# Kernel optimization log

Hardware: AMD Instinct MI355X
Metric: run time of the kernel (lower is better)

Reference implementation:

```python
import jax, jax.numpy as jnp
import numpy as np

ITER = 50
SMOOTH = 1e-05


def _max_pool(x, window):
    # x: [B, C, D, H, W]; 'same' max pool with stride 1, -inf padding
    # (matches torch F.max_pool3d semantics with symmetric padding).
    win = (1, 1) + window
    pads = [(0, 0), (0, 0)] + [((w - 1) // 2, (w - 1) // 2) for w in window]
    return jax.lax.reduce_window(x, -jnp.inf, jax.lax.max, win, (1,) * 5, pads)


def soft_erode(img):
    p1 = -_max_pool(-img, (3, 1, 1))
    p2 = -_max_pool(-img, (1, 3, 1))
    p3 = -_max_pool(-img, (1, 1, 3))
    return jnp.minimum(jnp.minimum(p1, p2), p3)


def soft_dilate(img):
    return _max_pool(img, (3, 3, 3))


def soft_open(img):
    return soft_dilate(soft_erode(img))


def soft_skel(img, n_iter):
    skel = jax.nn.relu(img - soft_open(img))

    def body(_, carry):
        img, skel = carry
        img = soft_erode(img)
        delta = jax.nn.relu(img - soft_open(img))
        skel = skel + jax.nn.relu(delta - skel * delta)
        return (img, skel)

    _, skel = jax.lax.fori_loop(0, n_iter, body, (img, skel))
    return skel


def setup_inputs() -> dict:
    key = jax.random.key(0)
    k1, k2 = jax.random.split(key)
    shape = (2, 2, 96, 192, 192)
    pred = jax.random.uniform(k1, shape, dtype=jnp.float32)
    target = jax.random.uniform(k2, shape, dtype=jnp.float32)
    return {"pred": pred, "target": target}


def reference(pred, target):
    pred_fg = pred[:, 1:2, ...]
    target_fg = target[:, 1:2, ...].astype(jnp.float32)
    skel_pred = soft_skel(pred_fg, ITER)
    skel_target = soft_skel(target_fg, ITER)
    tprec = (jnp.sum(skel_pred * target_fg) + SMOOTH) / (jnp.sum(skel_pred) + SMOOTH)
    tsens = (jnp.sum(skel_target * pred_fg) + SMOOTH) / (jnp.sum(skel_target) + SMOOTH)
    cl_dice = 2.0 * (tprec * tsens) / (tprec + tsens + SMOOTH)
    return 1.0 - cl_dice
```

## Files before the change

### kernel.cpp

```cpp
#include <hip/hip_runtime.h>
#include <math.h>

#define NX 192
#define NY 192
#define NZ 96
#define NV 4
#define VOL (NZ * NY * NX)
#define NTOT (NV * VOL)
#define YS NX
#define ZS (NY * NX)

#define TX 48
#define TY 16
#define ZCH 24
#define NG 14
#define AROWS (TY + 4)
#define EROWS (TY + 2)
#define AJOBS (AROWS * NG)
#define EJOBS (EROWS * NG)
#define UJOBS (TY * (TX / 4))

#define TY2 12
#define ZCH2 16
#define R2A 18

#define SLOT5(x) (((x) + 100) % 5)
#define SLOT3(x) (((x) + 99) % 3)
#define SLOT2(x) (((x) + 100) % 2)

#define HINF  0x7C00u
#define HNINF 0xFC00u

typedef _Float16 h2v __attribute__((ext_vector_type(2)));

struct __align__(8) H4u { unsigned lo, hi; };

__device__ __forceinline__ h2v h2_of(unsigned u) { return __builtin_bit_cast(h2v, u); }
__device__ __forceinline__ unsigned u_of(h2v h) { return __builtin_bit_cast(unsigned, h); }

__device__ __forceinline__ H4u h4min(H4u a, H4u b) {
    H4u r;
    r.lo = u_of(__builtin_elementwise_min(h2_of(a.lo), h2_of(b.lo)));
    r.hi = u_of(__builtin_elementwise_min(h2_of(a.hi), h2_of(b.hi)));
    return r;
}
__device__ __forceinline__ H4u h4max(H4u a, H4u b) {
    H4u r;
    r.lo = u_of(__builtin_elementwise_max(h2_of(a.lo), h2_of(b.lo)));
    r.hi = u_of(__builtin_elementwise_max(h2_of(a.hi), h2_of(b.hi)));
    return r;
}
__device__ __forceinline__ H4u shl1(H4u c, unsigned p16) {
    H4u r;
    r.lo = (c.lo << 16) | (p16 & 0xFFFFu);
    r.hi = (c.hi << 16) | (c.lo >> 16);
    return r;
}
__device__ __forceinline__ H4u shr1(H4u c, unsigned n16) {
    H4u r;
    r.lo = (c.lo >> 16) | (c.hi << 16);
    r.hi = (c.hi >> 16) | ((n16 & 0xFFFFu) << 16);
    return r;
}
__device__ __forceinline__ H4u f4_to_h4(float4 f) {
    h2v a, b;
    a[0] = (_Float16)f.x; a[1] = (_Float16)f.y;
    b[0] = (_Float16)f.z; b[1] = (_Float16)f.w;
    H4u r; r.lo = u_of(a); r.hi = u_of(b); return r;
}
__device__ __forceinline__ float4 h4_to_f4(H4u h) {
    h2v a = h2_of(h.lo), b = h2_of(h.hi);
    return make_float4((float)a[0], (float)a[1], (float)b[0], (float)b[1]);
}

__device__ __forceinline__ float4 min4(float4 a, float4 b) {
    return make_float4(fminf(a.x, b.x), fminf(a.y, b.y),
                       fminf(a.z, b.z), fminf(a.w, b.w));
}
__device__ __forceinline__ float4 max4(float4 a, float4 b) {
    return make_float4(fmaxf(a.x, b.x), fmaxf(a.y, b.y),
                       fmaxf(a.z, b.z), fmaxf(a.w, b.w));
}
__device__ __forceinline__ float4 win3max(float a, float4 b, float c) {
    return make_float4(fmaxf(fmaxf(a, b.x), b.y),
                       fmaxf(fmaxf(b.x, b.y), b.z),
                       fmaxf(fmaxf(b.y, b.z), b.w),
                       fmaxf(fmaxf(b.z, b.w), c));
}

template<bool FIRST>
__global__ __launch_bounds__(256, 6) void fused2_kernel(
    const float* __restrict__ pred, const float* __restrict__ target,
    const _Float16* __restrict__ Ain, _Float16* __restrict__ Eout,
    _Float16* __restrict__ skel)
{
    __shared__ H4u As[5][R2A][NG];
    __shared__ H4u E1c[3][16][NG];
    __shared__ H4u ZM1[2][16][NG];
    __shared__ H4u ZM2[2][16][NG];

    const int tid = threadIdx.x;
    const int lr  = tid >> 4;
    const int c   = tid & 15;
    const int cc  = (c < 14) ? c : 13;
    const int sr  = tid / 14;
    const int sg  = tid - sr * 14;

    const int x0 = blockIdx.x * TX;
    const int y0 = blockIdx.y * TY2;
    const int v  = blockIdx.z / 6;
    const int ch = blockIdx.z % 6;
    const int z0 = ch * ZCH2;
    const int z1 = z0 + ZCH2;

    const float* Af = nullptr;
    const _Float16* Ah = nullptr;
    if (FIRST) Af = ((v < 2) ? pred : target) + (size_t)((v & 1) * 2 + 1) * VOL;
    else       Ah = Ain + (size_t)v * VOL;
    _Float16* Ev = Eout + (size_t)v * VOL;
    _Float16* Sv = skel + (size_t)v * VOL;

    const H4u HP4 = { 0x7C007C00u, 0x7C007C00u };
    const H4u HN4 = { 0xFC00FC00u, 0xFC00FC00u };
    const float4 ZERO4 = make_float4(0.f, 0.f, 0.f, 0.f);

    const bool xlo = (x0 == 0);
    const bool xhi = (x0 + TX == NX);

    const int  gys  = y0 - 3 + sr;
    const int  gxs  = x0 - 4 + 4 * sg;
    const bool stIn = (sr < R2A) && (gys >= 0) && (gys < NY) &&
                      (gxs >= 0) && (gxs < NX);

    const int  gx   = x0 - 4 + 4 * c;
    const bool gxin = (c < 14) && (gx >= 0) && (gx < NX);
    const int  gyo  = y0 - 2 + lr;
    const bool yIn  = (gyo >= 0) && (gyo < NY);
    const bool uAct = (lr >= 2 && lr <= 13 && c >= 1 && c <= 12);
    const int  rdn  = (lr > 0) ? lr - 1 : 0;
    const int  rup  = (lr < 15) ? lr + 1 : 15;

    auto stageLoad = [&](int za) -> H4u {
        H4u val = HP4;
        if (stIn && za >= 0 && za < NZ) {
            if (FIRST)
                val = f4_to_h4(*(const float4*)(Af + (size_t)za * ZS + gys * YS + gxs));
            else
                val = *(const H4u*)(Ah + (size_t)za * ZS + gys * YS + gxs);
        }
        return val;
    };
    auto stageWrite = [&](int za, H4u val) {
        if (sr < R2A) As[SLOT5(za)][sr][sg] = val;
    };

    auto e1compute = [&](int zp) -> H4u {
        if (zp >= NZ) return HP4;
        const int s_c = SLOT5(zp), s_m = SLOT5(zp - 1), s_p = SLOT5(zp + 1);
        const bool hp = (zp + 1 < NZ);
        const int ar = lr + 1;
        H4u cen = As[s_c][ar][cc];
        H4u ylo = As[s_c][ar - 1][cc];
        H4u yhi = As[s_c][ar + 1][cc];
        H4u zlo = As[s_m][ar][cc];
        H4u zhi = hp ? As[s_p][ar][cc] : HP4;
        unsigned lw = __shfl_up(cen.hi, 1) >> 16;
        unsigned rx = __shfl_down(cen.lo, 1) & 0xFFFFu;
        if (c == 0) lw = HINF;
        H4u m = h4min(cen, shl1(cen, lw));
        m = h4min(m, shr1(cen, rx));
        m = h4min(m, h4min(ylo, yhi));
        m = h4min(m, h4min(zlo, zhi));
        if (zp < 0 || !yIn || !gxin) m = HP4;
        if (c < 14) E1c[SLOT3(zp)][lr][c] = m;
        return m;
    };

    stageWrite(z0 - 3, stageLoad(z0 - 3));
    stageWrite(z0 - 2, stageLoad(z0 - 2));
    stageWrite(z0 - 1, stageLoad(z0 - 1));
    stageWrite(z0,     stageLoad(z0));
    stageWrite(z0 + 1, stageLoad(z0 + 1));
    __syncthreads();
    H4u e1m2 = e1compute(z0 - 2);
    H4u e1m1 = e1compute(z0 - 1);
    __syncthreads();
    stageWrite(z0 + 2, stageLoad(z0 + 2));
    H4u e1c = e1compute(z0);
    __syncthreads();

    H4u e1m3 = HP4;
    H4u e2c = HN4, e2m1 = HN4;
    H4u zm1_prev = HN4, zm2_prev = HN4;
    float4 skA = ZERO4, sq1 = ZERO4, sq2 = ZERO4;

    for (int z = z0; z <= z1 + 2; ++z) {
        const bool doStage = (z <= z1 - 1);
        H4u stv = doStage ? stageLoad(z + 3) : HP4;
        float4 skN = ZERO4;
        if (!FIRST && z < z1 && uAct)
            skN = h4_to_f4(*(const H4u*)(Sv + (size_t)z * ZS + gyo * YS + gx));

        H4u e1new = (z + 1 <= z1 + 1) ? e1compute(z + 1) : HP4;

        H4u zm1w;
        {
            H4u t0 = (z >= 1) ? e1m1 : HN4;
            H4u t2 = (z + 1 < NZ) ? e1new : HN4;
            zm1w = h4max(t0, h4max(e1c, t2));
            if (!yIn || !gxin) zm1w = HN4;
            if (c < 14) ZM1[SLOT2(z)][lr][c] = zm1w;
        }

        const int p = z - 1;
        H4u e2new = HN4;
        if (p >= 0 && p <= z1 && p < NZ) {
            H4u cen = e1m1;
            H4u zlo = e1m2;
            H4u zhi = e1c;
            H4u ylo = E1c[SLOT3(p)][rdn][cc];
            H4u yhi = E1c[SLOT3(p)][rup][cc];
            unsigned lwE = __shfl_up(cen.hi, 1) >> 16;
            unsigned rxE = __shfl_down(cen.lo, 1) & 0xFFFFu;
            if (c == 0) lwE = HINF;
            H4u m2 = h4min(cen, shl1(cen, lwE));
            m2 = h4min(m2, shr1(cen, rxE));
            m2 = h4min(m2, h4min(ylo, yhi));
            m2 = h4min(m2, h4min(zlo, zhi));
            if (yIn && gxin) {
                e2new = m2;
                if (p >= z0 && p < z1 && lr >= 2 && lr <= 13 && c >= 1 && c <= 12)
                    *(H4u*)(Ev + (size_t)p * ZS + gyo * YS + gx) = m2;
            }
        }

        H4u zm2w = h4max(e2m1, h4max(e2c, e2new));
        if (c < 14) ZM2[SLOT2(z - 2)][lr][c] = zm2w;

        float4 spnew = ZERO4;
        if (p >= z0 && p < z1) {
            H4u vm = h4max(ZM1[SLOT2(p)][rdn][cc],
                     h4max(zm1_prev, ZM1[SLOT2(p)][rup][cc]));
            unsigned lw = __shfl_up(vm.hi, 1) >> 16;
            unsigned rx = __shfl_down(vm.lo, 1) & 0xFFFFu;
            if (xlo && c == 1)  lw = HNINF;
            if (xhi && c == 12) rx = HNINF;
            if (uAct) {
                H4u dilh = h4max(h4max(shl1(vm, lw), vm), shr1(vm, rx));
                float4 dil = h4_to_f4(dilh);
                float4 a = h4_to_f4(As[SLOT5(p)][lr + 1][cc]);
                float4 s = skA;
                float dd;
                dd = fmaxf(a.x - dil.x, 0.f); s.x += fmaxf(dd - s.x * dd, 0.f);
                dd = fmaxf(a.y - dil.y, 0.f); s.y += fmaxf(dd - s.y * dd, 0.f);
                dd = fmaxf(a.z - dil.z, 0.f); s.z += fmaxf(dd - s.z * dd, 0.f);
                dd = fmaxf(a.w - dil.w, 0.f); s.w += fmaxf(dd - s.w * dd, 0.f);
                spnew = s;
            }
        }

        const int q = z - 3;
        if (q >= z0 && q < z1) {
            H4u vm2 = h4max(ZM2[SLOT2(q)][rdn][cc],
                      h4max(zm2_prev, ZM2[SLOT2(q)][rup][cc]));
            unsigned lw = __shfl_up(vm2.hi, 1) >> 16;
            unsigned rx = __shfl_down(vm2.lo, 1) & 0xFFFFu;
            if (xlo && c == 1)  lw = HNINF;
            if (xhi && c == 12) rx = HNINF;
            if (uAct) {
                H4u dilh = h4max(h4max(shl1(vm2, lw), vm2), shr1(vm2, rx));
                float4 dil = h4_to_f4(dilh);
                float4 a = h4_to_f4(e1m3);
                float4 s = sq2;
                float dd;
                dd = fmaxf(a.x - dil.x, 0.f); s.x += fmaxf(dd - s.x * dd, 0.f);
                dd = fmaxf(a.y - dil.y, 0.f); s.y += fmaxf(dd - s.y * dd, 0.f);
                dd = fmaxf(a.z - dil.z, 0.f); s.z += fmaxf(dd - s.z * dd, 0.f);
                dd = fmaxf(a.w - dil.w, 0.f); s.w += fmaxf(dd - s.w * dd, 0.f);
                *(H4u*)(Sv + (size_t)q * ZS + gyo * YS + gx) = f4_to_h4(s);
            }
        }

        if (doStage) stageWrite(z + 3, stv);

        __syncthreads();
        e1m3 = e1m2; e1m2 = e1m1; e1m1 = e1c; e1c = e1new;
        e2m1 = e2c; e2c = e2new;
        zm1_prev = zm1w; zm2_prev = zm2w;
        sq2 = sq1; sq1 = spnew; skA = skN;
    }
}

__global__ __launch_bounds__(256, 3) void fused_last_kernel(
    const _Float16* __restrict__ Ain,
    const float* __restrict__ pred, const float* __restrict__ target,
    const _Float16* __restrict__ skel, double* __restrict__ sums)
{
    __shared__ float4 As[4][AROWS][NG];
    __shared__ float4 Es[3][EROWS][NG];
    __shared__ float4 Ms[EROWS][NG];
    __shared__ double sred[8];

    const int tid = threadIdx.x;
    const int x0 = blockIdx.x * TX;
    const int y0 = blockIdx.y * TY;
    const int v  = blockIdx.z >> 2;
    const int z0 = (blockIdx.z & 3) * ZCH;
    const int z1 = z0 + ZCH;

    const _Float16* Av = Ain + (size_t)v * VOL;
    const _Float16* Sv = skel + (size_t)v * VOL;
    const float* Ov = ((v < 2) ? target : pred) + (size_t)((v & 1) * 2 + 1) * VOL;

    const float4 PINF4 = make_float4(INFINITY, INFINITY, INFINITY, INFINITY);
    const float4 NINF4 = make_float4(-INFINITY, -INFINITY, -INFINITY, -INFINITY);
    const float4 ZERO4 = make_float4(0.f, 0.f, 0.f, 0.f);

    const int ur  = tid / (TX / 4);
    const int ugp = tid - ur * (TX / 4);

    auto stageA = [&](int z) {
        int slot = (z + 8) & 3;
        float4* dst = &As[slot][0][0];
        if (z < 0 || z >= NZ) {
            for (int j = tid; j < AJOBS; j += 256) dst[j] = PINF4;
        } else {
            const _Float16* P = Av + (size_t)z * ZS;
            for (int j = tid; j < AJOBS; j += 256) {
                int r = j / NG, g = j - r * NG;
                int gy = y0 - 2 + r;
                int gx0 = x0 - 4 + 4 * g;
                float4 val = PINF4;
                if (gy >= 0 && gy < NY && gx0 >= 0 && gx0 < NX)
                    val = h4_to_f4(*(const H4u*)(P + gy * YS + gx0));
                dst[j] = val;
            }
        }
    };

    auto eplane = [&](int z) {
        int es = (z + 9) % 3;
        float4* dst = &Es[es][0][0];
        if (z < 0 || z >= NZ) {
            for (int j = tid; j < EJOBS; j += 256) dst[j] = NINF4;
            return;
        }
        const int sc = (z + 8) & 3;
        const int sm = (z + 7) & 3;
        const int sp = (z + 9) & 3;
        for (int j = tid; j < EJOBS; j += 256) {
            int r = j / NG, g = j - r * NG;
            float4 c  = As[sc][r + 1][g];
            float4 yl = As[sc][r][g];
            float4 yh = As[sc][r + 2][g];
            float4 zl = As[sm][r + 1][g];
            float4 zh = As[sp][r + 1][g];
            float pw = (g > 0)      ? As[sc][r + 1][g - 1].w : INFINITY;
            float nx = (g < NG - 1) ? As[sc][r + 1][g + 1].x : INFINITY;
            float4 xl = make_float4(pw, c.x, c.y, c.z);
            float4 xr = make_float4(c.y, c.z, c.w, nx);
            float4 m = min4(c, xl);
            m = min4(m, xr);
            m = min4(m, yl);
            m = min4(m, yh);
            m = min4(m, zl);
            m = min4(m, zh);
            int gy = y0 - 1 + r;
            int gx0 = x0 - 4 + 4 * g;
            if (gy < 0 || gy >= NY || gx0 < 0 || gx0 >= NX) m = NINF4;
            dst[j] = m;
        }
    };

    stageA(z0 - 2); stageA(z0 - 1); stageA(z0); stageA(z0 + 1);
    __syncthreads();
    eplane(z0 - 1);
    eplane(z0);
    __syncthreads();
    stageA(z0 + 2);
    __syncthreads();

    double afd = 0.0, afs = 0.0;

    for (int z = z0; z < z1; ++z) {
        float4 oCur = ZERO4;
        if (tid < UJOBS)
            oCur = *(const float4*)(Ov + (size_t)z * ZS +
                                    (size_t)(y0 + ur) * YS + (x0 + ugp * 4));
        stageA(z + 3);
        eplane(z + 1);
        __syncthreads();
        {
            const float4* e0 = &Es[(z + 8) % 3][0][0];
            const float4* e1 = &Es[(z + 9) % 3][0][0];
            const float4* e2 = &Es[(z + 10) % 3][0][0];
            float4* mm = &Ms[0][0];
            for (int j = tid; j < EJOBS; j += 256)
                mm[j] = max4(max4(e0[j], e1[j]), e2[j]);
        }
        __syncthreads();
        if (tid < UJOBS) {
            int g = ugp + 1;
            float4 d = NINF4;
#pragma unroll
            for (int dy = 0; dy < 3; ++dy) {
                float a  = Ms[ur + dy][g - 1].w;
                float4 b = Ms[ur + dy][g];
                float cx = Ms[ur + dy][g + 1].x;
                d = max4(d, win3max(a, b, cx));
            }
            float4 av = As[(z + 8) & 3][ur + 2][g];
            float4 delta = make_float4(fmaxf(av.x - d.x, 0.0f),
                                       fmaxf(av.y - d.y, 0.0f),
                                       fmaxf(av.z - d.z, 0.0f),
                                       fmaxf(av.w - d.w, 0.0f));
            size_t gi = (size_t)z * ZS + (size_t)(y0 + ur) * YS + (x0 + ugp * 4);
            float4 s = h4_to_f4(*(const H4u*)(Sv + gi));
            s.x += fmaxf(delta.x - s.x * delta.x, 0.0f);
            s.y += fmaxf(delta.y - s.y * delta.y, 0.0f);
            s.z += fmaxf(delta.z - s.z * delta.z, 0.0f);
            s.w += fmaxf(delta.w - s.w * delta.w, 0.0f);
            afd += (double)(s.x * oCur.x + s.y * oCur.y +
                            s.z * oCur.z + s.w * oCur.w);
            afs += (double)(s.x + s.y + s.z + s.w);
        }
        __syncthreads();
    }

#pragma unroll
    for (int off = 32; off > 0; off >>= 1) {
        afd += __shfl_down(afd, off, 64);
        afs += __shfl_down(afs, off, 64);
    }
    int lane = tid & 63, wid = tid >> 6;
    if (lane == 0) { sred[wid * 2] = afd; sred[wid * 2 + 1] = afs; }
    __syncthreads();
    if (tid == 0) {
        double fd = sred[0] + sred[2] + sred[4] + sred[6];
        double fs = sred[1] + sred[3] + sred[5] + sred[7];
        if (v < 2) { atomicAdd(&sums[0], fd); atomicAdd(&sums[1], fs); }
        else       { atomicAdd(&sums[2], fd); atomicAdd(&sums[3], fs); }
    }
}

__global__ void final_kernel(const double* __restrict__ sums,
                             float* __restrict__ out) {
    if (threadIdx.x == 0 && blockIdx.x == 0) {
        const double SM = 1e-5;
        double tprec = (sums[0] + SM) / (sums[1] + SM);
        double tsens = (sums[2] + SM) / (sums[3] + SM);
        double cl = 2.0 * tprec * tsens / (tprec + tsens + SM);
        out[0] = (float)(1.0 - cl);
    }
}

extern "C" void kernel_launch(void* const* d_in, const int* in_sizes, int n_in,
                              void* d_out, int out_size, void* d_ws, size_t ws_size,
                              hipStream_t stream) {
    const float* pred = (const float*)d_in[0];
    const float* target = (const float*)d_in[1];
    float* out = (float*)d_out;

    _Float16* H0 = (_Float16*)d_ws;
    _Float16* H1 = H0 + NTOT;
    _Float16* skel = H1 + NTOT;
    double* sums = (double*)(skel + NTOT);

    hipMemsetAsync(sums, 0, 4 * sizeof(double), stream);

    dim3 dgrid(NX / TX, NY / TY2, NV * 6);
    dim3 fgrid(NX / TX, NY / TY, NV * 4);

    fused2_kernel<true><<<dgrid, 256, 0, stream>>>(pred, target, H0, H0, skel);
    _Float16* A = H0;
    _Float16* B = H1;
    for (int j = 0; j < 24; ++j) {
        fused2_kernel<false><<<dgrid, 256, 0, stream>>>(pred, target, A, B, skel);
        _Float16* t = A; A = B; B = t;
    }
    fused_last_kernel<<<fgrid, 256, 0, stream>>>(A, pred, target, skel, sums);

    final_kernel<<<1, 64, 0, stream>>>(sums, out);
}
```

Baseline: 1.705 ms.

## Compute skeleton update in packed fp16 and rewrite last kernel as register-streaming

```diff
diff --git a/kernel.cpp b/kernel.cpp
--- a/kernel.cpp
+++ b/kernel.cpp
@@ -11,20 +11,12 @@
 #define ZS (NY * NX)
 
 #define TX 48
-#define TY 16
-#define ZCH 24
-#define NG 14
-#define AROWS (TY + 4)
-#define EROWS (TY + 2)
-#define AJOBS (AROWS * NG)
-#define EJOBS (EROWS * NG)
-#define UJOBS (TY * (TX / 4))
-
 #define TY2 12
 #define ZCH2 16
+#define NG 14
 #define R2A 18
 
-#define SLOT5(x) (((x) + 100) % 5)
+#define SLOT4(x) (((x) + 100) % 4)
 #define SLOT3(x) (((x) + 99) % 3)
 #define SLOT2(x) (((x) + 100) % 2)
 
@@ -49,6 +41,31 @@
     r.lo = u_of(__builtin_elementwise_max(h2_of(a.lo), h2_of(b.lo)));
     r.hi = u_of(__builtin_elementwise_max(h2_of(a.hi), h2_of(b.hi)));
     return r;
+}
+__device__ __forceinline__ H4u h4add(H4u a, H4u b) {
+    H4u r;
+    r.lo = u_of(h2_of(a.lo) + h2_of(b.lo));
+    r.hi = u_of(h2_of(a.hi) + h2_of(b.hi));
+    return r;
+}
+__device__ __forceinline__ H4u h4sub(H4u a, H4u b) {
+    H4u r;
+    r.lo = u_of(h2_of(a.lo) - h2_of(b.lo));
+    r.hi = u_of(h2_of(a.hi) - h2_of(b.hi));
+    return r;
+}
+__device__ __forceinline__ H4u h4mul(H4u a, H4u b) {
+    H4u r;
+    r.lo = u_of(h2_of(a.lo) * h2_of(b.lo));
+    r.hi = u_of(h2_of(a.hi) * h2_of(b.hi));
+    return r;
+}
+__device__ __forceinline__ H4u h4skel(H4u s, H4u a, H4u dil) {
+    const H4u HZ4 = { 0u, 0u };
+    const H4u HONE = { 0x3C003C00u, 0x3C003C00u };
+    H4u dd = h4max(h4sub(a, dil), HZ4);
+    H4u t = h4mul(dd, h4sub(HONE, s));
+    return h4add(s, h4max(t, HZ4));
 }
 __device__ __forceinline__ H4u shl1(H4u c, unsigned p16) {
     H4u r;
@@ -71,21 +88,6 @@
 __device__ __forceinline__ float4 h4_to_f4(H4u h) {
     h2v a = h2_of(h.lo), b = h2_of(h.hi);
     return make_float4((float)a[0], (float)a[1], (float)b[0], (float)b[1]);
-}
-
-__device__ __forceinline__ float4 min4(float4 a, float4 b) {
-    return make_float4(fminf(a.x, b.x), fminf(a.y, b.y),
-                       fminf(a.z, b.z), fminf(a.w, b.w));
-}
-__device__ __forceinline__ float4 max4(float4 a, float4 b) {
-    return make_float4(fmaxf(a.x, b.x), fmaxf(a.y, b.y),
-                       fmaxf(a.z, b.z), fmaxf(a.w, b.w));
-}
-__device__ __forceinline__ float4 win3max(float a, float4 b, float c) {
-    return make_float4(fmaxf(fmaxf(a, b.x), b.y),
-                       fmaxf(fmaxf(b.x, b.y), b.z),
-                       fmaxf(fmaxf(b.y, b.z), b.w),
-                       fmaxf(fmaxf(b.z, b.w), c));
 }
 
 template<bool FIRST>
@@ -94,7 +96,7 @@
     const _Float16* __restrict__ Ain, _Float16* __restrict__ Eout,
     _Float16* __restrict__ skel)
 {
-    __shared__ H4u As[5][R2A][NG];
+    __shared__ H4u As[4][R2A][NG];
     __shared__ H4u E1c[3][16][NG];
     __shared__ H4u ZM1[2][16][NG];
     __shared__ H4u ZM2[2][16][NG];
@@ -122,7 +124,7 @@
 
     const H4u HP4 = { 0x7C007C00u, 0x7C007C00u };
     const H4u HN4 = { 0xFC00FC00u, 0xFC00FC00u };
-    const float4 ZERO4 = make_float4(0.f, 0.f, 0.f, 0.f);
+    const H4u HZ4 = { 0u, 0u };
 
     const bool xlo = (x0 == 0);
     const bool xhi = (x0 + TX == NX);
@@ -151,12 +153,12 @@
         return val;
     };
     auto stageWrite = [&](int za, H4u val) {
-        if (sr < R2A) As[SLOT5(za)][sr][sg] = val;
-    };
-
-    auto e1compute = [&](int zp) -> H4u {
-        if (zp >= NZ) return HP4;
-        const int s_c = SLOT5(zp), s_m = SLOT5(zp - 1), s_p = SLOT5(zp + 1);
+        if (sr < R2A) As[SLOT4(za)][sr][sg] = val;
+    };
+
+    auto e1compute = [&](int zp, H4u& cenOut) -> H4u {
+        if (zp >= NZ) { cenOut = HP4; return HP4; }
+        const int s_c = SLOT4(zp), s_m = SLOT4(zp - 1), s_p = SLOT4(zp + 1);
         const bool hp = (zp + 1 < NZ);
         const int ar = lr + 1;
         H4u cen = As[s_c][ar][cc];
@@ -164,6 +166,7 @@
         H4u yhi = As[s_c][ar + 1][cc];
         H4u zlo = As[s_m][ar][cc];
         H4u zhi = hp ? As[s_p][ar][cc] : HP4;
+        cenOut = cen;
         unsigned lw = __shfl_up(cen.hi, 1) >> 16;
         unsigned rx = __shfl_down(cen.lo, 1) & 0xFFFFu;
         if (c == 0) lw = HINF;
@@ -180,28 +183,31 @@
     stageWrite(z0 - 2, stageLoad(z0 - 2));
     stageWrite(z0 - 1, stageLoad(z0 - 1));
     stageWrite(z0,     stageLoad(z0));
+    __syncthreads();
+    H4u aT, a1, a2 = HP4;
+    H4u e1m2 = e1compute(z0 - 2, aT);
+    H4u e1m1 = e1compute(z0 - 1, aT);
+    __syncthreads();
     stageWrite(z0 + 1, stageLoad(z0 + 1));
     __syncthreads();
-    H4u e1m2 = e1compute(z0 - 2);
-    H4u e1m1 = e1compute(z0 - 1);
-    __syncthreads();
+    H4u e1c = e1compute(z0, a1);
     stageWrite(z0 + 2, stageLoad(z0 + 2));
-    H4u e1c = e1compute(z0);
     __syncthreads();
 
     H4u e1m3 = HP4;
     H4u e2c = HN4, e2m1 = HN4;
     H4u zm1_prev = HN4, zm2_prev = HN4;
-    float4 skA = ZERO4, sq1 = ZERO4, sq2 = ZERO4;
+    H4u skA = HZ4, sq1 = HZ4, sq2 = HZ4;
 
     for (int z = z0; z <= z1 + 2; ++z) {
         const bool doStage = (z <= z1 - 1);
         H4u stv = doStage ? stageLoad(z + 3) : HP4;
-        float4 skN = ZERO4;
+        H4u skN = HZ4;
         if (!FIRST && z < z1 && uAct)
-            skN = h4_to_f4(*(const H4u*)(Sv + (size_t)z * ZS + gyo * YS + gx));
-
-        H4u e1new = (z + 1 <= z1 + 1) ? e1compute(z + 1) : HP4;
+            skN = *(const H4u*)(Sv + (size_t)z * ZS + gyo * YS + gx);
+
+        H4u aC = HP4;
+        H4u e1new = (z <= z1) ? e1compute(z + 1, aC) : HP4;
 
         H4u zm1w;
         {
@@ -237,7 +243,7 @@
         H4u zm2w = h4max(e2m1, h4max(e2c, e2new));
         if (c < 14) ZM2[SLOT2(z - 2)][lr][c] = zm2w;
 
-        float4 spnew = ZERO4;
+        H4u spnew = HZ4;
         if (p >= z0 && p < z1) {
             H4u vm = h4max(ZM1[SLOT2(p)][rdn][cc],
                      h4max(zm1_prev, ZM1[SLOT2(p)][rup][cc]));
@@ -247,15 +253,7 @@
             if (xhi && c == 12) rx = HNINF;
             if (uAct) {
                 H4u dilh = h4max(h4max(shl1(vm, lw), vm), shr1(vm, rx));
-                float4 dil = h4_to_f4(dilh);
-                float4 a = h4_to_f4(As[SLOT5(p)][lr + 1][cc]);
-                float4 s = skA;
-                float dd;
-                dd = fmaxf(a.x - dil.x, 0.f); s.x += fmaxf(dd - s.x * dd, 0.f);
-                dd = fmaxf(a.y - dil.y, 0.f); s.y += fmaxf(dd - s.y * dd, 0.f);
-                dd = fmaxf(a.z - dil.z, 0.f); s.z += fmaxf(dd - s.z * dd, 0.f);
-                dd = fmaxf(a.w - dil.w, 0.f); s.w += fmaxf(dd - s.w * dd, 0.f);
-                spnew = s;
+                spnew = h4skel(skA, a2, dilh);
             }
         }
 
@@ -269,15 +267,8 @@
             if (xhi && c == 12) rx = HNINF;
             if (uAct) {
                 H4u dilh = h4max(h4max(shl1(vm2, lw), vm2), shr1(vm2, rx));
-                float4 dil = h4_to_f4(dilh);
-                float4 a = h4_to_f4(e1m3);
-                float4 s = sq2;
-                float dd;
-                dd = fmaxf(a.x - dil.x, 0.f); s.x += fmaxf(dd - s.x * dd, 0.f);
-                dd = fmaxf(a.y - dil.y, 0.f); s.y += fmaxf(dd - s.y * dd, 0.f);
-                dd = fmaxf(a.z - dil.z, 0.f); s.z += fmaxf(dd - s.z * dd, 0.f);
-                dd = fmaxf(a.w - dil.w, 0.f); s.w += fmaxf(dd - s.w * dd, 0.f);
-                *(H4u*)(Sv + (size_t)q * ZS + gyo * YS + gx) = f4_to_h4(s);
+                H4u s = h4skel(sq2, e1m3, dilh);
+                *(H4u*)(Sv + (size_t)q * ZS + gyo * YS + gx) = s;
             }
         }
 
@@ -287,144 +278,155 @@
         e1m3 = e1m2; e1m2 = e1m1; e1m1 = e1c; e1c = e1new;
         e2m1 = e2c; e2c = e2new;
         zm1_prev = zm1w; zm2_prev = zm2w;
+        a2 = a1; a1 = aC;
         sq2 = sq1; sq1 = spnew; skA = skN;
     }
 }
 
-__global__ __launch_bounds__(256, 3) void fused_last_kernel(
+__global__ __launch_bounds__(256, 6) void last_kernel(
     const _Float16* __restrict__ Ain,
     const float* __restrict__ pred, const float* __restrict__ target,
     const _Float16* __restrict__ skel, double* __restrict__ sums)
 {
-    __shared__ float4 As[4][AROWS][NG];
-    __shared__ float4 Es[3][EROWS][NG];
-    __shared__ float4 Ms[EROWS][NG];
+    __shared__ H4u As[4][R2A][NG];
+    __shared__ H4u ZM1[2][16][NG];
     __shared__ double sred[8];
 
     const int tid = threadIdx.x;
+    const int lr  = tid >> 4;
+    const int c   = tid & 15;
+    const int cc  = (c < 14) ? c : 13;
+    const int sr  = tid / 14;
+    const int sg  = tid - sr * 14;
+
     const int x0 = blockIdx.x * TX;
-    const int y0 = blockIdx.y * TY;
-    const int v  = blockIdx.z >> 2;
-    const int z0 = (blockIdx.z & 3) * ZCH;
-    const int z1 = z0 + ZCH;
-
-    const _Float16* Av = Ain + (size_t)v * VOL;
+    const int y0 = blockIdx.y * TY2;
+    const int v  = blockIdx.z / 6;
+    const int ch = blockIdx.z % 6;
+    const int z0 = ch * ZCH2;
+    const int z1 = z0 + ZCH2;
+
+    const _Float16* Ah = Ain + (size_t)v * VOL;
     const _Float16* Sv = skel + (size_t)v * VOL;
     const float* Ov = ((v < 2) ? target : pred) + (size_t)((v & 1) * 2 + 1) * VOL;
 
-    const float4 PINF4 = make_float4(INFINITY, INFINITY, INFINITY, INFINITY);
-    const float4 NINF4 = make_float4(-INFINITY, -INFINITY, -INFINITY, -INFINITY);
+    const H4u HP4 = { 0x7C007C00u, 0x7C007C00u };
+    const H4u HN4 = { 0xFC00FC00u, 0xFC00FC00u };
+    const H4u HZ4 = { 0u, 0u };
     const float4 ZERO4 = make_float4(0.f, 0.f, 0.f, 0.f);
 
-    const int ur  = tid / (TX / 4);
-    const int ugp = tid - ur * (TX / 4);
-
-    auto stageA = [&](int z) {
-        int slot = (z + 8) & 3;
-        float4* dst = &As[slot][0][0];
-        if (z < 0 || z >= NZ) {
-            for (int j = tid; j < AJOBS; j += 256) dst[j] = PINF4;
-        } else {
-            const _Float16* P = Av + (size_t)z * ZS;
-            for (int j = tid; j < AJOBS; j += 256) {
-                int r = j / NG, g = j - r * NG;
-                int gy = y0 - 2 + r;
-                int gx0 = x0 - 4 + 4 * g;
-                float4 val = PINF4;
-                if (gy >= 0 && gy < NY && gx0 >= 0 && gx0 < NX)
-                    val = h4_to_f4(*(const H4u*)(P + gy * YS + gx0));
-                dst[j] = val;
+    const bool xlo = (x0 == 0);
+    const bool xhi = (x0 + TX == NX);
+
+    const int  gys  = y0 - 3 + sr;
+    const int  gxs  = x0 - 4 + 4 * sg;
+    const bool stIn = (sr < R2A) && (gys >= 0) && (gys < NY) &&
+                      (gxs >= 0) && (gxs < NX);
+
+    const int  gx   = x0 - 4 + 4 * c;
+    const bool gxin = (c < 14) && (gx >= 0) && (gx < NX);
+    const int  gyo  = y0 - 2 + lr;
+    const bool yIn  = (gyo >= 0) && (gyo < NY);
+    const bool uAct = (lr >= 2 && lr <= 13 && c >= 1 && c <= 12);
+    const int  rdn  = (lr > 0) ? lr - 1 : 0;
+    const int  rup  = (lr < 15) ? lr + 1 : 15;
+
+    auto stageLoad = [&](int za) -> H4u {
+        H4u val = HP4;
+        if (stIn && za >= 0 && za < NZ)
+            val = *(const H4u*)(Ah + (size_t)za * ZS + gys * YS + gxs);
+        return val;
+    };
+    auto stageWrite = [&](int za, H4u val) {
+        if (sr < R2A) As[SLOT4(za)][sr][sg] = val;
+    };
+
+    auto e1compute = [&](int zp, H4u& cenOut) -> H4u {
+        if (zp >= NZ) { cenOut = HP4; return HP4; }
+        const int s_c = SLOT4(zp), s_m = SLOT4(zp - 1), s_p = SLOT4(zp + 1);
+        const bool hp = (zp + 1 < NZ);
+        const int ar = lr + 1;
+        H4u cen = As[s_c][ar][cc];
+        H4u ylo = As[s_c][ar - 1][cc];
+        H4u yhi = As[s_c][ar + 1][cc];
+        H4u zlo = As[s_m][ar][cc];
+        H4u zhi = hp ? As[s_p][ar][cc] : HP4;
+        cenOut = cen;
+        unsigned lw = __shfl_up(cen.hi, 1) >> 16;
+        unsigned rx = __shfl_down(cen.lo, 1) & 0xFFFFu;
+        if (c == 0) lw = HINF;
+        H4u m = h4min(cen, shl1(cen, lw));
+        m = h4min(m, shr1(cen, rx));
+        m = h4min(m, h4min(ylo, yhi));
+        m = h4min(m, h4min(zlo, zhi));
+        if (zp < 0 || !yIn || !gxin) m = HP4;
+        return m;
+    };
+
+    stageWrite(z0 - 2, stageLoad(z0 - 2));
+    stageWrite(z0 - 1, stageLoad(z0 - 1));
+    stageWrite(z0,     stageLoad(z0));
+    stageWrite(z0 + 1, stageLoad(z0 + 1));
+    __syncthreads();
+    H4u aT, a1, a2 = HP4;
+    H4u e1m1 = e1compute(z0 - 1, aT);
+    H4u e1c  = e1compute(z0, a1);
+    __syncthreads();
+    stageWrite(z0 + 2, stageLoad(z0 + 2));
+    __syncthreads();
+
+    H4u zmP = HN4;
+    H4u skA = HZ4;
+    float4 oA = ZERO4;
+    double afd = 0.0, afs = 0.0;
+
+    for (int z = z0; z <= z1; ++z) {
+        const bool doStage = (z <= z1 - 2);
+        H4u stv = doStage ? stageLoad(z + 3) : HP4;
+        H4u skN = HZ4;
+        float4 oN = ZERO4;
+        if (z < z1 && uAct) {
+            skN = *(const H4u*)(Sv + (size_t)z * ZS + gyo * YS + gx);
+            oN  = *(const float4*)(Ov + (size_t)z * ZS + gyo * YS + gx);
+        }
+
+        H4u aC = HP4;
+        H4u e1new = (z + 1 <= z1) ? e1compute(z + 1, aC) : HP4;
+
+        H4u zm1w = HN4;
+        if (z <= z1 - 1) {
+            H4u t0 = (z >= 1) ? e1m1 : HN4;
+            H4u t2 = (z + 1 < NZ) ? e1new : HN4;
+            zm1w = h4max(t0, h4max(e1c, t2));
+            if (!yIn || !gxin) zm1w = HN4;
+            if (c < 14) ZM1[SLOT2(z)][lr][c] = zm1w;
+        }
+
+        const int p = z - 1;
+        if (p >= z0 && p < z1) {
+            H4u vm = h4max(ZM1[SLOT2(p)][rdn][cc],
+                     h4max(zmP, ZM1[SLOT2(p)][rup][cc]));
+            unsigned lw = __shfl_up(vm.hi, 1) >> 16;
+            unsigned rx = __shfl_down(vm.lo, 1) & 0xFFFFu;
+            if (xlo && c == 1)  lw = HNINF;
+            if (xhi && c == 12) rx = HNINF;
+            if (uAct) {
+                H4u dilh = h4max(h4max(shl1(vm, lw), vm), shr1(vm, rx));
+                H4u s = h4skel(skA, a2, dilh);
+                float4 sf = h4_to_f4(s);
+                afd += (double)(sf.x * oA.x + sf.y * oA.y +
+                                sf.z * oA.z + sf.w * oA.w);
+                afs += (double)(sf.x + sf.y + sf.z + sf.w);
             }
         }
-    };
-
-    auto eplane = [&](int z) {
-        int es = (z + 9) % 3;
-        float4* dst = &Es[es][0][0];
-        if (z < 0 || z >= NZ) {
-            for (int j = tid; j < EJOBS; j += 256) dst[j] = NINF4;
-            return;
-        }
-        const int sc = (z + 8) & 3;
-        const int sm = (z + 7) & 3;
-        const int sp = (z + 9) & 3;
-        for (int j = tid; j < EJOBS; j += 256) {
-            int r = j / NG, g = j - r * NG;
-            float4 c  = As[sc][r + 1][g];
-            float4 yl = As[sc][r][g];
-            float4 yh = As[sc][r + 2][g];
-            float4 zl = As[sm][r + 1][g];
-            float4 zh = As[sp][r + 1][g];
-            float pw = (g > 0)      ? As[sc][r + 1][g - 1].w : INFINITY;
-            float nx = (g < NG - 1) ? As[sc][r + 1][g + 1].x : INFINITY;
-            float4 xl = make_float4(pw, c.x, c.y, c.z);
-            float4 xr = make_float4(c.y, c.z, c.w, nx);
-            float4 m = min4(c, xl);
-            m = min4(m, xr);
-            m = min4(m, yl);
-            m = min4(m, yh);
-            m = min4(m, zl);
-            m = min4(m, zh);
-            int gy = y0 - 1 + r;
-            int gx0 = x0 - 4 + 4 * g;
-            if (gy < 0 || gy >= NY || gx0 < 0 || gx0 >= NX) m = NINF4;
-            dst[j] = m;
-        }
-    };
-
-    stageA(z0 - 2); stageA(z0 - 1); stageA(z0); stageA(z0 + 1);
-    __syncthreads();
-    eplane(z0 - 1);
-    eplane(z0);
-    __syncthreads();
-    stageA(z0 + 2);
-    __syncthreads();
-
-    double afd = 0.0, afs = 0.0;
-
-    for (int z = z0; z < z1; ++z) {
-        float4 oCur = ZERO4;
-        if (tid < UJOBS)
-            oCur = *(const float4*)(Ov + (size_t)z * ZS +
-                                    (size_t)(y0 + ur) * YS + (x0 + ugp * 4));
-        stageA(z + 3);
-        eplane(z + 1);
+
+        if (doStage) stageWrite(z + 3, stv);
+
         __syncthreads();
-        {
-            const float4* e0 = &Es[(z + 8) % 3][0][0];
-            const float4* e1 = &Es[(z + 9) % 3][0][0];
-            const float4* e2 = &Es[(z + 10) % 3][0][0];
-            float4* mm = &Ms[0][0];
-            for (int j = tid; j < EJOBS; j += 256)
-                mm[j] = max4(max4(e0[j], e1[j]), e2[j]);
-        }
-        __syncthreads();
-        if (tid < UJOBS) {
-            int g = ugp + 1;
-            float4 d = NINF4;
-#pragma unroll
-            for (int dy = 0; dy < 3; ++dy) {
-                float a  = Ms[ur + dy][g - 1].w;
-                float4 b = Ms[ur + dy][g];
-                float cx = Ms[ur + dy][g + 1].x;
-                d = max4(d, win3max(a, b, cx));
-            }
-            float4 av = As[(z + 8) & 3][ur + 2][g];
-            float4 delta = make_float4(fmaxf(av.x - d.x, 0.0f),
-                                       fmaxf(av.y - d.y, 0.0f),
-                                       fmaxf(av.z - d.z, 0.0f),
-                                       fmaxf(av.w - d.w, 0.0f));
-            size_t gi = (size_t)z * ZS + (size_t)(y0 + ur) * YS + (x0 + ugp * 4);
-            float4 s = h4_to_f4(*(const H4u*)(Sv + gi));
-            s.x += fmaxf(delta.x - s.x * delta.x, 0.0f);
-            s.y += fmaxf(delta.y - s.y * delta.y, 0.0f);
-            s.z += fmaxf(delta.z - s.z * delta.z, 0.0f);
-            s.w += fmaxf(delta.w - s.w * delta.w, 0.0f);
-            afd += (double)(s.x * oCur.x + s.y * oCur.y +
-                            s.z * oCur.z + s.w * oCur.w);
-            afs += (double)(s.x + s.y + s.z + s.w);
-        }
-        __syncthreads();
+        e1m1 = e1c; e1c = e1new;
+        a2 = a1; a1 = aC;
+        zmP = zm1w;
+        skA = skN; oA = oN;
     }
 
 #pragma unroll
@@ -469,7 +471,6 @@
     hipMemsetAsync(sums, 0, 4 * sizeof(double), stream);
 
     dim3 dgrid(NX / TX, NY / TY2, NV * 6);
-    dim3 fgrid(NX / TX, NY / TY, NV * 4);
 
     fused2_kernel<true><<<dgrid, 256, 0, stream>>>(pred, target, H0, H0, skel);
     _Float16* A = H0;
@@ -478,7 +479,7 @@
         fused2_kernel<false><<<dgrid, 256, 0, stream>>>(pred, target, A, B, skel);
         _Float16* t = A; A = B; B = t;
     }
-    fused_last_kernel<<<fgrid, 256, 0, stream>>>(A, pred, target, skel, sums);
+    last_kernel<<<dgrid, 256, 0, stream>>>(A, pred, target, skel, sums);
 
     final_kernel<<<1, 64, 0, stream>>>(sums, out);
 }
```

Result: faster. 1.444 ms (-15.3%).
